# Kernel tuning notes

Measured on AMD Instinct MI355X. Metric: run time of the kernel, lower is better.

Reference implementation:

```python
import jax, jax.numpy as jnp
import numpy as np

N, E, IN, H, OUT, CD = 50000, 800000, 64, 128, 128, 2


def _lin(key, fi, fo):
    # PyTorch nn.Linear default init: U(-1/sqrt(fan_in), 1/sqrt(fan_in))
    k1, k2 = jax.random.split(key)
    s = 1.0 / np.sqrt(fi)
    W = jax.random.uniform(k1, (fi, fo), minval=-s, maxval=s, dtype=jnp.float32)
    b = jax.random.uniform(k2, (fo,), minval=-s, maxval=s, dtype=jnp.float32)
    return W, b


def setup_inputs() -> dict:
    key = jax.random.key(0)
    ks = jax.random.split(key, 12)
    feat = jax.random.normal(ks[0], (N, IN), dtype=jnp.float32)
    offsets = jax.random.normal(ks[1], (E, CD), dtype=jnp.float32)
    src = jax.random.randint(ks[2], (E,), 0, N)
    dst = jax.random.randint(ks[3], (E,), 0, N)
    kW1, kb1 = _lin(ks[4], CD, H)
    kW2, kb2 = _lin(ks[5], H, IN)
    sW1, sb1 = _lin(ks[6], IN, H)
    sW2, sb2 = _lin(ks[7], H, H)
    mW1, mb1 = _lin(ks[8], IN + H, H)
    mW2, mb2 = _lin(ks[9], H, H)
    mW3, mb3 = _lin(ks[10], H, H)
    mW4, mb4 = _lin(ks[11], H, OUT)
    return dict(feat=feat, offsets=offsets, src=src, dst=dst,
                kW1=kW1, kb1=kb1, kW2=kW2, kb2=kb2,
                sW1=sW1, sb1=sb1, sW2=sW2, sb2=sb2,
                mW1=mW1, mb1=mb1, mW2=mW2, mb2=mb2,
                mW3=mW3, mb3=mb3, mW4=mW4, mb4=mb4)


def reference(feat, offsets, src, dst, kW1, kb1, kW2, kb2, sW1, sb1, sW2, sb2,
              mW1, mb1, mW2, mb2, mW3, mb3, mW4, mb4):
    elu = jax.nn.elu
    n = feat.shape[0]
    # per-edge kernel weights from offsets: [E, IN]
    kw = elu(offsets @ kW1 + kb1) @ kW2 + kb2
    # dist_fn == 'eculidean': score = 1 / (||offsets||_1 + 0.001), edge softmax per dst node
    score = 1.0 / (jnp.sum(jnp.abs(offsets), axis=1) + 0.001)  # [E]
    mx = jax.lax.stop_gradient(jax.ops.segment_max(score, dst, num_segments=n))
    ex = jnp.exp(score - mx[dst])
    w = ex / jax.ops.segment_sum(ex, dst, num_segments=n)[dst]  # [E]
    # u_mul_e + sum aggregation: gather src feats, scale by per-edge weights, scatter-add to dst
    m = feat[src] * (w[:, None] * kw)                     # [E, IN]
    agg = jax.ops.segment_sum(m, dst, num_segments=n)     # [N, IN]
    # self branch
    h_self = elu(feat @ sW1 + sb1) @ sW2 + sb2            # [N, H]
    # concat + MLP head
    h = jnp.concatenate([agg, h_self], axis=1)            # [N, IN+H]
    h = elu(h @ mW1 + mb1)
    h = elu(h @ mW2 + mb2)
    h = elu(h @ mW3 + mb3)
    return h @ mW4 + mb4                                  # [N, OUT]
```

## Files before the change

kernel.cpp:

```cpp
#include <hip/hip_runtime.h>
#include <hip/hip_bf16.h>
#include <math.h>

#define N_NODES 50000
#define N_EDGES 800000
#define NB_SCAN ((N_NODES + 255) / 256)

typedef _Float16 half8 __attribute__((ext_vector_type(8)));
typedef _Float16 half4 __attribute__((ext_vector_type(4)));
typedef float f32x4 __attribute__((ext_vector_type(4)));

__device__ __forceinline__ float elu_f(float x) { return x > 0.f ? x : __expf(x) - 1.f; }
__device__ __forceinline__ float edge_score(float2 o) {
    return 1.f / (fabsf(o.x) + fabsf(o.y) + 0.001f);
}

__global__ __launch_bounds__(256)
void k_deg(const int* __restrict__ dst, int* __restrict__ deg) {
    int e = blockIdx.x * 256 + threadIdx.x;
    if (e >= N_EDGES) return;
    atomicAdd(&deg[dst[e]], 1);
}

__global__ __launch_bounds__(256)
void k_bsum(const int* __restrict__ deg, int* __restrict__ bsum) {
    int i = blockIdx.x * 256 + threadIdx.x;
    int v = (i < N_NODES) ? deg[i] : 0;
    #pragma unroll
    for (int d = 32; d; d >>= 1) v += __shfl_xor(v, d);
    __shared__ int ws[4];
    if ((threadIdx.x & 63) == 0) ws[threadIdx.x >> 6] = v;
    __syncthreads();
    if (threadIdx.x == 0) bsum[blockIdx.x] = ws[0] + ws[1] + ws[2] + ws[3];
}

__global__ __launch_bounds__(256)
void k_bscan(const int* __restrict__ bsum, int* __restrict__ bpre, int* __restrict__ rs) {
    const int t = threadIdx.x, lane = t & 63, wv = t >> 6;
    int v = (t < NB_SCAN) ? bsum[t] : 0;
    int inc = v;
    #pragma unroll
    for (int d = 1; d < 64; d <<= 1) { int u = __shfl_up(inc, d); if (lane >= d) inc += u; }
    __shared__ int wtot[4];
    if (lane == 63) wtot[wv] = inc;
    __syncthreads();
    int add = 0;
    for (int w = 0; w < wv; ++w) add += wtot[w];
    if (t < NB_SCAN) bpre[t] = inc + add - v;
    if (t == 0) rs[N_NODES] = N_EDGES;
}

__global__ __launch_bounds__(256)
void k_wr(const int* __restrict__ deg, const int* __restrict__ bpre,
          int* __restrict__ rs, int* __restrict__ cur) {
    const int i = blockIdx.x * 256 + threadIdx.x;
    const int lane = threadIdx.x & 63, wv = threadIdx.x >> 6;
    int v = (i < N_NODES) ? deg[i] : 0;
    int inc = v;
    #pragma unroll
    for (int d = 1; d < 64; d <<= 1) { int u = __shfl_up(inc, d); if (lane >= d) inc += u; }
    __shared__ int wtot[4];
    if (lane == 63) wtot[wv] = inc;
    __syncthreads();
    int add = bpre[blockIdx.x];
    for (int w = 0; w < wv; ++w) add += wtot[w];
    if (i < N_NODES) { int excl = inc - v + add; rs[i] = excl; cur[i] = excl; }
}

__global__ __launch_bounds__(256)
void k_fill(const int* __restrict__ dst, const int* __restrict__ src,
            const float* __restrict__ off2, int* __restrict__ cur,
            int* __restrict__ perm, int* __restrict__ src_csr,
            float* __restrict__ score_csr) {
    int e = blockIdx.x * 256 + threadIdx.x;
    if (e >= N_EDGES) return;
    int p = atomicAdd(&cur[dst[e]], 1);
    perm[e] = p;
    src_csr[p] = src[e];
    score_csr[p] = edge_score(((const float2*)off2)[e]);
}

#define WTOT 98304
__global__ __launch_bounds__(256)
void k_wsplit(const float* __restrict__ sW1, const float* __restrict__ sW2,
              const float* __restrict__ mW1, const float* __restrict__ mW2,
              const float* __restrict__ mW3, const float* __restrict__ mW4,
              _Float16* __restrict__ wsH, _Float16* __restrict__ wsL) {
    int idx = blockIdx.x * 256 + threadIdx.x;
    if (idx >= WTOT) return;
    const float* W; int base, K;
    if      (idx < 8192)  { W = sW1; base = 0;     K = 64;  }
    else if (idx < 24576) { W = sW2; base = 8192;  K = 128; }
    else if (idx < 49152) { W = mW1; base = 24576; K = 192; }
    else if (idx < 65536) { W = mW2; base = 49152; K = 128; }
    else if (idx < 81920) { W = mW3; base = 65536; K = 128; }
    else                  { W = mW4; base = 81920; K = 128; }
    int local = idx - base;
    int k = local >> 7, col = local & 127;
    int nt = col >> 4, colg = col & 15;
    int kt = k >> 5, lq = (k >> 3) & 3, i = k & 7;
    int fi = base + ((nt * (K >> 5) + kt) * 4 + lq) * 128 + colg * 8 + i;
    float w = W[k * 128 + col];
    _Float16 h = (_Float16)w;
    wsH[fi] = h;
    wsL[fi] = (_Float16)(w - (float)h);
}

#define KW2TOT 8192
__global__ __launch_bounds__(256)
void k_kwsplit2(const float* __restrict__ kW2,
                _Float16* __restrict__ wkH, _Float16* __restrict__ wkL) {
    int idx = blockIdx.x * 256 + threadIdx.x;
    if (idx >= KW2TOT) return;
    int i = idx & 7, colg = (idx >> 3) & 15;
    int lq = (idx >> 7) & 3, kt = (idx >> 9) & 3, jt = idx >> 11;
    int k = kt * 32 + lq * 8 + i;
    int j = jt * 16 + colg;
    float w = kW2[k * 64 + j];
    _Float16 h = (_Float16)w;
    wkH[idx] = h;
    wkL[idx] = (_Float16)(w - (float)h);
}

__global__ __launch_bounds__(256)
void k_kw(const float* __restrict__ off2,
          const float* __restrict__ kW1, const float* __restrict__ kb1,
          const _Float16* __restrict__ wkH, const _Float16* __restrict__ wkL,
          const float* __restrict__ kb2, const int* __restrict__ perm,
          _Float16* __restrict__ kwbuf) {
    const int t = threadIdx.x;
    const int lane = t & 63, wv = t >> 6;
    const int eb = blockIdx.x * 256 + wv * 64;
    const int colg = lane & 15, lq = lane >> 4;

    float2 o[4];
    int pidx[4];
    #pragma unroll
    for (int et = 0; et < 4; ++et) {
        o[et] = ((const float2*)off2)[eb + et * 16 + colg];
        pidx[et] = perm[eb + et * 16 + colg];
    }

    f32x4 c[4][4];
    #pragma unroll
    for (int et = 0; et < 4; ++et)
        #pragma unroll
        for (int jt = 0; jt < 4; ++jt) c[et][jt] = (f32x4){0.f, 0.f, 0.f, 0.f};

    #pragma unroll
    for (int kt = 0; kt < 4; ++kt) {
        const int k0 = kt * 32 + lq * 8;
        float4 a0 = *(const float4*)&kW1[k0];
        float4 a1 = *(const float4*)&kW1[k0 + 4];
        float4 b0 = *(const float4*)&kW1[128 + k0];
        float4 b1 = *(const float4*)&kW1[128 + k0 + 4];
        float4 c0 = *(const float4*)&kb1[k0];
        float4 c1 = *(const float4*)&kb1[k0 + 4];
        const float wa[8] = {a0.x, a0.y, a0.z, a0.w, a1.x, a1.y, a1.z, a1.w};
        const float wb[8] = {b0.x, b0.y, b0.z, b0.w, b1.x, b1.y, b1.z, b1.w};
        const float bb[8] = {c0.x, c0.y, c0.z, c0.w, c1.x, c1.y, c1.z, c1.w};

        half8 Bh[4], Bl[4];
        #pragma unroll
        for (int et = 0; et < 4; ++et) {
            #pragma unroll
            for (int i = 0; i < 8; ++i) {
                float h = elu_f(fmaf(o[et].y, wb[i], fmaf(o[et].x, wa[i], bb[i])));
                _Float16 hh = (_Float16)h;
                Bh[et][i] = hh;
                Bl[et][i] = (_Float16)(h - (float)hh);
            }
        }
        #pragma unroll
        for (int jt = 0; jt < 4; ++jt) {
            int fo = ((jt * 4 + kt) * 4 + lq) * 128 + colg * 8;
            half8 Ah = *(const half8*)&wkH[fo];
            half8 Al = *(const half8*)&wkL[fo];
            #pragma unroll
            for (int et = 0; et < 4; ++et) {
                c[et][jt] = __builtin_amdgcn_mfma_f32_16x16x32_f16(Ah, Bh[et], c[et][jt], 0, 0, 0);
                c[et][jt] = __builtin_amdgcn_mfma_f32_16x16x32_f16(Ah, Bl[et], c[et][jt], 0, 0, 0);
                c[et][jt] = __builtin_amdgcn_mfma_f32_16x16x32_f16(Al, Bh[et], c[et][jt], 0, 0, 0);
            }
        }
    }

    #pragma unroll
    for (int jt = 0; jt < 4; ++jt) {
        const int j0 = jt * 16 + lq * 4;
        float4 bv = *(const float4*)&kb2[j0];
        const float bias4[4] = {bv.x, bv.y, bv.z, bv.w};
        #pragma unroll
        for (int et = 0; et < 4; ++et) {
            half4 v;
            #pragma unroll
            for (int r = 0; r < 4; ++r) v[r] = (_Float16)(c[et][jt][r] + bias4[r]);
            *(half4*)&kwbuf[(size_t)pidx[et] * 64 + j0] = v;
        }
    }
}

__global__ __launch_bounds__(256)
void k_agg(const float* __restrict__ score_csr, const int* __restrict__ src_csr,
           const int* __restrict__ rs, const float* __restrict__ feat,
           const _Float16* __restrict__ kwbuf, float* __restrict__ agg) {
    const int lane = threadIdx.x & 63;
    const int wav  = threadIdx.x >> 6;
    const int gw   = blockIdx.x * 4 + wav;
    const int nw   = gridDim.x * 4;

    for (int n = gw; n < N_NODES; n += nw) {
        const int p0 = rs[n], p1 = rs[n + 1];
        if (p0 == p1) { agg[(size_t)n * 64 + lane] = 0.f; continue; }

        float mx = 0.f;
        for (int p = p0 + lane; p < p1; p += 64) mx = fmaxf(mx, score_csr[p]);
        #pragma unroll
        for (int d = 32; d; d >>= 1) mx = fmaxf(mx, __shfl_xor(mx, d));

        float sm = 0.f;
        for (int p = p0 + lane; p < p1; p += 64) sm += __expf(score_csr[p] - mx);
        #pragma unroll
        for (int d = 32; d; d >>= 1) sm += __shfl_xor(sm, d);
        const float dinv = 1.f / sm;

        float a0 = 0.f, a1 = 0.f, a2 = 0.f, a3 = 0.f;
        int p = p0;
        for (; p + 4 <= p1; p += 4) {
            float w0 = __expf(score_csr[p]     - mx) * dinv;
            float w1 = __expf(score_csr[p + 1] - mx) * dinv;
            float w2 = __expf(score_csr[p + 2] - mx) * dinv;
            float w3 = __expf(score_csr[p + 3] - mx) * dinv;
            const int s0 = src_csr[p], s1 = src_csr[p + 1];
            const int s2 = src_csr[p + 2], s3 = src_csr[p + 3];
            float f0 = feat[(size_t)s0 * 64 + lane];
            float f1 = feat[(size_t)s1 * 64 + lane];
            float f2 = feat[(size_t)s2 * 64 + lane];
            float f3 = feat[(size_t)s3 * 64 + lane];
            float k0 = (float)kwbuf[(size_t)(p)     * 64 + lane];
            float k1 = (float)kwbuf[(size_t)(p + 1) * 64 + lane];
            float k2 = (float)kwbuf[(size_t)(p + 2) * 64 + lane];
            float k3 = (float)kwbuf[(size_t)(p + 3) * 64 + lane];
            a0 = fmaf(f0 * w0, k0, a0);
            a1 = fmaf(f1 * w1, k1, a1);
            a2 = fmaf(f2 * w2, k2, a2);
            a3 = fmaf(f3 * w3, k3, a3);
        }
        for (; p < p1; ++p) {
            float wgt = __expf(score_csr[p] - mx) * dinv;
            float f = feat[(size_t)src_csr[p] * 64 + lane];
            float kv = (float)kwbuf[(size_t)p * 64 + lane];
            a0 = fmaf(f * wgt, kv, a0);
        }
        agg[(size_t)n * 64 + lane] = (a0 + a1) + (a2 + a3);
    }
}

__device__ __forceinline__
void mm64(const char* XH, const char* XL, const _Float16* __restrict__ WH,
          const _Float16* __restrict__ WL, int K, int lane, int wv, f32x4 c[4][2]) {
    const int colg = lane & 15, lq = lane >> 4;
    #pragma unroll
    for (int m = 0; m < 4; ++m)
        #pragma unroll
        for (int j = 0; j < 2; ++j) c[m][j] = (f32x4){0.f, 0.f, 0.f, 0.f};
    const int KT = K >> 5;
    for (int kt = 0; kt < KT; ++kt) {
        half8 Bh[2], Bl[2], Ah[4], Al[4];
        #pragma unroll
        for (int j = 0; j < 2; ++j) {
            int fo = ((((wv * 2 + j) * KT + kt) * 4 + lq) * 128) + colg * 8;
            Bh[j] = *(const half8*)&WH[fo];
            Bl[j] = *(const half8*)&WL[fo];
        }
        #pragma unroll
        for (int m = 0; m < 4; ++m) {
            int row = m * 16 + colg;
            int byte = ((row * K + kt * 32 + lq * 8) * 2) ^ ((row & 7) << 4);
            Ah[m] = *(const half8*)(XH + byte);
            Al[m] = *(const half8*)(XL + byte);
        }
        #pragma unroll
        for (int m = 0; m < 4; ++m)
            #pragma unroll
            for (int j = 0; j < 2; ++j) {
                c[m][j] = __builtin_amdgcn_mfma_f32_16x16x32_f16(Ah[m], Bh[j], c[m][j], 0, 0, 0);
                c[m][j] = __builtin_amdgcn_mfma_f32_16x16x32_f16(Ah[m], Bl[j], c[m][j], 0, 0, 0);
                c[m][j] = __builtin_amdgcn_mfma_f32_16x16x32_f16(Al[m], Bh[j], c[m][j], 0, 0, 0);
            }
    }
}

__device__ __forceinline__
void epi_lds(char* XH, char* XL, int Knext, int colOff, int lane, int wv,
             f32x4 c[4][2], const float* __restrict__ bias, bool do_elu) {
    const int colg = lane & 15, lq = lane >> 4;
    float bj[2] = { bias[wv * 32 + colg], bias[wv * 32 + 16 + colg] };
    #pragma unroll
    for (int m = 0; m < 4; ++m)
        #pragma unroll
        for (int j = 0; j < 2; ++j) {
            int col = colOff + wv * 32 + j * 16 + colg;
            #pragma unroll
            for (int r = 0; r < 4; ++r) {
                int row = m * 16 + lq * 4 + r;
                float v = c[m][j][r] + bj[j];
                if (do_elu) v = elu_f(v);
                _Float16 h = (_Float16)v;
                int byte = ((row * Knext + col) * 2) ^ ((row & 7) << 4);
                *(_Float16*)(XH + byte) = h;
                *(_Float16*)(XL + byte) = (_Float16)(v - (float)h);
            }
        }
}

__global__ __launch_bounds__(256)
void k_node(const float* __restrict__ feat, const float* __restrict__ agg,
            const _Float16* __restrict__ wsH, const _Float16* __restrict__ wsL,
            const float* __restrict__ sb1, const float* __restrict__ sb2,
            const float* __restrict__ mb1, const float* __restrict__ mb2,
            const float* __restrict__ mb3, const float* __restrict__ mb4,
            float* __restrict__ out) {
    __shared__ _Float16 XH[64 * 192];
    __shared__ _Float16 XL[64 * 192];
    const int t = threadIdx.x;
    const int lane = t & 63, wv = t >> 6;
    const int row0 = blockIdx.x * 64;
    f32x4 c[4][2];

    {
        int r = t >> 2, c4 = (t & 3) * 4;
        #pragma unroll
        for (int q = 0; q < 4; ++q) {
            int col = (c4 + q) * 4;
            float4 v = make_float4(0.f, 0.f, 0.f, 0.f);
            if (row0 + r < N_NODES) v = *(const float4*)&feat[(size_t)(row0 + r) * 64 + col];
            _Float16 h4h[4], h4l[4];
            float vv[4] = {v.x, v.y, v.z, v.w};
            #pragma unroll
            for (int i = 0; i < 4; ++i) {
                _Float16 h = (_Float16)vv[i];
                h4h[i] = h; h4l[i] = (_Float16)(vv[i] - (float)h);
            }
            int byte = ((r * 64 + col) * 2) ^ ((r & 7) << 4);
            *(ulong1*)((char*)XH + byte) = *(ulong1*)h4h;
            *(ulong1*)((char*)XL + byte) = *(ulong1*)h4l;
        }
    }
    __syncthreads();

    mm64((const char*)XH, (const char*)XL, wsH + 0, wsL + 0, 64, lane, wv, c);
    __syncthreads();
    epi_lds((char*)XH, (char*)XL, 128, 0, lane, wv, c, sb1, true);
    __syncthreads();

    mm64((const char*)XH, (const char*)XL, wsH + 8192, wsL + 8192, 128, lane, wv, c);
    __syncthreads();
    epi_lds((char*)XH, (char*)XL, 192, 64, lane, wv, c, sb2, false);
    {
        int r = t >> 2, c4 = (t & 3) * 4;
        #pragma unroll
        for (int q = 0; q < 4; ++q) {
            int col = (c4 + q) * 4;
            float4 v = make_float4(0.f, 0.f, 0.f, 0.f);
            if (row0 + r < N_NODES) v = *(const float4*)&agg[(size_t)(row0 + r) * 64 + col];
            _Float16 h4h[4], h4l[4];
            float vv[4] = {v.x, v.y, v.z, v.w};
            #pragma unroll
            for (int i = 0; i < 4; ++i) {
                _Float16 h = (_Float16)vv[i];
                h4h[i] = h; h4l[i] = (_Float16)(vv[i] - (float)h);
            }
            int byte = ((r * 192 + col) * 2) ^ ((r & 7) << 4);
            *(ulong1*)((char*)XH + byte) = *(ulong1*)h4h;
            *(ulong1*)((char*)XL + byte) = *(ulong1*)h4l;
        }
    }
    __syncthreads();

    mm64((const char*)XH, (const char*)XL, wsH + 24576, wsL + 24576, 192, lane, wv, c);
    __syncthreads();
    epi_lds((char*)XH, (char*)XL, 128, 0, lane, wv, c, mb1, true);
    __syncthreads();

    mm64((const char*)XH, (const char*)XL, wsH + 49152, wsL + 49152, 128, lane, wv, c);
    __syncthreads();
    epi_lds((char*)XH, (char*)XL, 128, 0, lane, wv, c, mb2, true);
    __syncthreads();

    mm64((const char*)XH, (const char*)XL, wsH + 65536, wsL + 65536, 128, lane, wv, c);
    __syncthreads();
    epi_lds((char*)XH, (char*)XL, 128, 0, lane, wv, c, mb3, true);
    __syncthreads();

    mm64((const char*)XH, (const char*)XL, wsH + 81920, wsL + 81920, 128, lane, wv, c);
    {
        const int colg = lane & 15, lq = lane >> 4;
        float bj[2] = { mb4[wv * 32 + colg], mb4[wv * 32 + 16 + colg] };
        #pragma unroll
        for (int m = 0; m < 4; ++m)
            #pragma unroll
            for (int j = 0; j < 2; ++j) {
                int col = wv * 32 + j * 16 + colg;
                #pragma unroll
                for (int r = 0; r < 4; ++r) {
                    int row = row0 + m * 16 + lq * 4 + r;
                    if (row < N_NODES)
                        out[(size_t)row * 128 + col] = c[m][j][r] + bj[j];
                }
            }
    }
}

extern "C" void kernel_launch(void* const* d_in, const int* in_sizes, int n_in,
                              void* d_out, int out_size, void* d_ws, size_t ws_size,
                              hipStream_t stream) {
    (void)in_sizes; (void)n_in; (void)out_size; (void)ws_size;
    const float* feat = (const float*)d_in[0];
    const float* off2 = (const float*)d_in[1];
    const int*   src  = (const int*)d_in[2];
    const int*   dst  = (const int*)d_in[3];
    const float* kW1  = (const float*)d_in[4];
    const float* kb1  = (const float*)d_in[5];
    const float* kW2  = (const float*)d_in[6];
    const float* kb2  = (const float*)d_in[7];
    const float* sW1  = (const float*)d_in[8];
    const float* sb1  = (const float*)d_in[9];
    const float* sW2  = (const float*)d_in[10];
    const float* sb2  = (const float*)d_in[11];
    const float* mW1  = (const float*)d_in[12];
    const float* mb1  = (const float*)d_in[13];
    const float* mW2  = (const float*)d_in[14];
    const float* mb2  = (const float*)d_in[15];
    const float* mW3  = (const float*)d_in[16];
    const float* mb3  = (const float*)d_in[17];
    const float* mW4  = (const float*)d_in[18];
    const float* mb4  = (const float*)d_in[19];

    char* ws = (char*)d_ws;
    size_t off = 0;
    auto alloc = [&](size_t bytes) -> void* {
        void* p = ws + off;
        off += (bytes + 255) & ~(size_t)255;
        return p;
    };
    int*   deg    = (int*)alloc((size_t)N_NODES * 4);
    int*   rs     = (int*)alloc((size_t)(N_NODES + 8) * 4);
    int*   cur    = (int*)alloc((size_t)N_NODES * 4);
    int*   bsum   = (int*)alloc((size_t)NB_SCAN * 4);
    int*   bpre   = (int*)alloc((size_t)NB_SCAN * 4);
    int*   perm   = (int*)alloc((size_t)N_EDGES * 4);
    int*   srcc   = (int*)alloc((size_t)N_EDGES * 4);
    float* scorec = (float*)alloc((size_t)N_EDGES * 4);
    float* agg    = (float*)alloc((size_t)N_NODES * 64 * 4);
    _Float16* wsH = (_Float16*)alloc((size_t)WTOT * 2);
    _Float16* wsL = (_Float16*)alloc((size_t)WTOT * 2);
    _Float16* wkH = (_Float16*)alloc((size_t)KW2TOT * 2);
    _Float16* wkL = (_Float16*)alloc((size_t)KW2TOT * 2);
    _Float16* kwbuf = (_Float16*)alloc((size_t)N_EDGES * 64 * 2);

    hipMemsetAsync(deg, 0, (size_t)N_NODES * 4, stream);

    const int EB = (N_EDGES + 255) / 256;
    const int GB = (N_NODES + 63) / 64;

    k_deg     <<<EB, 256, 0, stream>>>(dst, deg);
    k_bsum    <<<NB_SCAN, 256, 0, stream>>>(deg, bsum);
    k_bscan   <<<1, 256, 0, stream>>>(bsum, bpre, rs);
    k_wr      <<<NB_SCAN, 256, 0, stream>>>(deg, bpre, rs, cur);
    k_fill    <<<EB, 256, 0, stream>>>(dst, src, off2, cur, perm, srcc, scorec);
    k_wsplit  <<<(WTOT + 255) / 256, 256, 0, stream>>>(sW1, sW2, mW1, mW2, mW3, mW4, wsH, wsL);
    k_kwsplit2<<<(KW2TOT + 255) / 256, 256, 0, stream>>>(kW2, wkH, wkL);

    k_kw <<<N_EDGES / 256, 256, 0, stream>>>(off2, kW1, kb1, wkH, wkL, kb2, perm, kwbuf);
    k_agg<<<2048, 256, 0, stream>>>(scorec, srcc, rs, feat, kwbuf, agg);

    k_node<<<GB, 256, 0, stream>>>(feat, agg, wsH, wsL, sb1, sb2, mb1, mb2, mb3, mb4,
                                   (float*)d_out);
}
```

Measured before the change: 278.9 us.

## Use CSR edge-id gather in k_kw, merge weight-split kernels, keep agg in registers

k_fill now records the original edge id per CSR slot instead of a per-edge permutation. k_kw therefore gathers offsets through that id and writes kernel weights contiguously in CSR order, replacing scattered half4 stores with a gathered float2 load. The two weight-split kernels are merged into one launch. In k_node the aggregated features are loaded straight into MFMA operand registers for the first MLP layer, which shrinks LDS from 192 to 128 columns and drops a staging pass, at the cost of more registers.

```diff
diff --git a/kernel.cpp b/kernel.cpp
--- a/kernel.cpp
+++ b/kernel.cpp
@@ -70,76 +70,70 @@
 __global__ __launch_bounds__(256)
 void k_fill(const int* __restrict__ dst, const int* __restrict__ src,
             const float* __restrict__ off2, int* __restrict__ cur,
-            int* __restrict__ perm, int* __restrict__ src_csr,
+            int* __restrict__ eid_csr, int* __restrict__ src_csr,
             float* __restrict__ score_csr) {
     int e = blockIdx.x * 256 + threadIdx.x;
     if (e >= N_EDGES) return;
     int p = atomicAdd(&cur[dst[e]], 1);
-    perm[e] = p;
+    eid_csr[p] = e;
     src_csr[p] = src[e];
     score_csr[p] = edge_score(((const float2*)off2)[e]);
 }
 
 #define WTOT 98304
+#define KW2TOT 8192
 __global__ __launch_bounds__(256)
 void k_wsplit(const float* __restrict__ sW1, const float* __restrict__ sW2,
               const float* __restrict__ mW1, const float* __restrict__ mW2,
               const float* __restrict__ mW3, const float* __restrict__ mW4,
-              _Float16* __restrict__ wsH, _Float16* __restrict__ wsL) {
+              const float* __restrict__ kW2,
+              _Float16* __restrict__ wsH, _Float16* __restrict__ wsL,
+              _Float16* __restrict__ wkH, _Float16* __restrict__ wkL) {
     int idx = blockIdx.x * 256 + threadIdx.x;
-    if (idx >= WTOT) return;
-    const float* W; int base, K;
-    if      (idx < 8192)  { W = sW1; base = 0;     K = 64;  }
-    else if (idx < 24576) { W = sW2; base = 8192;  K = 128; }
-    else if (idx < 49152) { W = mW1; base = 24576; K = 192; }
-    else if (idx < 65536) { W = mW2; base = 49152; K = 128; }
-    else if (idx < 81920) { W = mW3; base = 65536; K = 128; }
-    else                  { W = mW4; base = 81920; K = 128; }
-    int local = idx - base;
-    int k = local >> 7, col = local & 127;
-    int nt = col >> 4, colg = col & 15;
-    int kt = k >> 5, lq = (k >> 3) & 3, i = k & 7;
-    int fi = base + ((nt * (K >> 5) + kt) * 4 + lq) * 128 + colg * 8 + i;
-    float w = W[k * 128 + col];
-    _Float16 h = (_Float16)w;
-    wsH[fi] = h;
-    wsL[fi] = (_Float16)(w - (float)h);
-}
-
-#define KW2TOT 8192
-__global__ __launch_bounds__(256)
-void k_kwsplit2(const float* __restrict__ kW2,
-                _Float16* __restrict__ wkH, _Float16* __restrict__ wkL) {
-    int idx = blockIdx.x * 256 + threadIdx.x;
-    if (idx >= KW2TOT) return;
-    int i = idx & 7, colg = (idx >> 3) & 15;
-    int lq = (idx >> 7) & 3, kt = (idx >> 9) & 3, jt = idx >> 11;
-    int k = kt * 32 + lq * 8 + i;
-    int j = jt * 16 + colg;
-    float w = kW2[k * 64 + j];
-    _Float16 h = (_Float16)w;
-    wkH[idx] = h;
-    wkL[idx] = (_Float16)(w - (float)h);
-}
-
-__global__ __launch_bounds__(256)
-void k_kw(const float* __restrict__ off2,
+    if (idx < WTOT) {
+        const float* W; int base, K;
+        if      (idx < 8192)  { W = sW1; base = 0;     K = 64;  }
+        else if (idx < 24576) { W = sW2; base = 8192;  K = 128; }
+        else if (idx < 49152) { W = mW1; base = 24576; K = 192; }
+        else if (idx < 65536) { W = mW2; base = 49152; K = 128; }
+        else if (idx < 81920) { W = mW3; base = 65536; K = 128; }
+        else                  { W = mW4; base = 81920; K = 128; }
+        int local = idx - base;
+        int k = local >> 7, col = local & 127;
+        int nt = col >> 4, colg = col & 15;
+        int kt = k >> 5, lq = (k >> 3) & 3, i = k & 7;
+        int fi = base + ((nt * (K >> 5) + kt) * 4 + lq) * 128 + colg * 8 + i;
+        float w = W[k * 128 + col];
+        _Float16 h = (_Float16)w;
+        wsH[fi] = h;
+        wsL[fi] = (_Float16)(w - (float)h);
+    } else if (idx < WTOT + KW2TOT) {
+        int x = idx - WTOT;
+        int i = x & 7, colg = (x >> 3) & 15;
+        int lq = (x >> 7) & 3, kt = (x >> 9) & 3, jt = x >> 11;
+        int k = kt * 32 + lq * 8 + i;
+        int j = jt * 16 + colg;
+        float w = kW2[k * 64 + j];
+        _Float16 h = (_Float16)w;
+        wkH[x] = h;
+        wkL[x] = (_Float16)(w - (float)h);
+    }
+}
+
+__global__ __launch_bounds__(256)
+void k_kw(const float* __restrict__ off2, const int* __restrict__ eid_csr,
           const float* __restrict__ kW1, const float* __restrict__ kb1,
           const _Float16* __restrict__ wkH, const _Float16* __restrict__ wkL,
-          const float* __restrict__ kb2, const int* __restrict__ perm,
-          _Float16* __restrict__ kwbuf) {
+          const float* __restrict__ kb2, _Float16* __restrict__ kwbuf) {
     const int t = threadIdx.x;
     const int lane = t & 63, wv = t >> 6;
-    const int eb = blockIdx.x * 256 + wv * 64;
+    const int pb = blockIdx.x * 256 + wv * 64;
     const int colg = lane & 15, lq = lane >> 4;
 
     float2 o[4];
-    int pidx[4];
-    #pragma unroll
-    for (int et = 0; et < 4; ++et) {
-        o[et] = ((const float2*)off2)[eb + et * 16 + colg];
-        pidx[et] = perm[eb + et * 16 + colg];
-    }
+    #pragma unroll
+    for (int et = 0; et < 4; ++et)
+        o[et] = ((const float2*)off2)[eid_csr[pb + et * 16 + colg]];
 
     f32x4 c[4][4];
     #pragma unroll
@@ -192,10 +186,11 @@
         const float bias4[4] = {bv.x, bv.y, bv.z, bv.w};
         #pragma unroll
         for (int et = 0; et < 4; ++et) {
+            const int p = pb + et * 16 + colg;
             half4 v;
             #pragma unroll
             for (int r = 0; r < 4; ++r) v[r] = (_Float16)(c[et][jt][r] + bias4[r]);
-            *(half4*)&kwbuf[(size_t)pidx[et] * 64 + j0] = v;
+            *(half4*)&kwbuf[(size_t)p * 64 + j0] = v;
         }
     }
 }
@@ -292,7 +287,49 @@
 }
 
 __device__ __forceinline__
-void epi_lds(char* XH, char* XL, int Knext, int colOff, int lane, int wv,
+void mm64_h1(const half8 aggH[4][2], const half8 aggL[4][2],
+             const char* XH, const char* XL,
+             const _Float16* __restrict__ WH, const _Float16* __restrict__ WL,
+             int lane, int wv, f32x4 c[4][2]) {
+    const int colg = lane & 15, lq = lane >> 4;
+    #pragma unroll
+    for (int m = 0; m < 4; ++m)
+        #pragma unroll
+        for (int j = 0; j < 2; ++j) c[m][j] = (f32x4){0.f, 0.f, 0.f, 0.f};
+    #pragma unroll
+    for (int kt = 0; kt < 6; ++kt) {
+        half8 Bh[2], Bl[2], Ah[4], Al[4];
+        #pragma unroll
+        for (int j = 0; j < 2; ++j) {
+            int fo = ((((wv * 2 + j) * 6 + kt) * 4 + lq) * 128) + colg * 8;
+            Bh[j] = *(const half8*)&WH[fo];
+            Bl[j] = *(const half8*)&WL[fo];
+        }
+        if (kt < 2) {
+            #pragma unroll
+            for (int m = 0; m < 4; ++m) { Ah[m] = aggH[m][kt]; Al[m] = aggL[m][kt]; }
+        } else {
+            #pragma unroll
+            for (int m = 0; m < 4; ++m) {
+                int row = m * 16 + colg;
+                int byte = ((row * 128 + (kt - 2) * 32 + lq * 8) * 2) ^ ((row & 7) << 4);
+                Ah[m] = *(const half8*)(XH + byte);
+                Al[m] = *(const half8*)(XL + byte);
+            }
+        }
+        #pragma unroll
+        for (int m = 0; m < 4; ++m)
+            #pragma unroll
+            for (int j = 0; j < 2; ++j) {
+                c[m][j] = __builtin_amdgcn_mfma_f32_16x16x32_f16(Ah[m], Bh[j], c[m][j], 0, 0, 0);
+                c[m][j] = __builtin_amdgcn_mfma_f32_16x16x32_f16(Ah[m], Bl[j], c[m][j], 0, 0, 0);
+                c[m][j] = __builtin_amdgcn_mfma_f32_16x16x32_f16(Al[m], Bh[j], c[m][j], 0, 0, 0);
+            }
+    }
+}
+
+__device__ __forceinline__
+void epi_lds(char* XH, char* XL, int lane, int wv,
              f32x4 c[4][2], const float* __restrict__ bias, bool do_elu) {
     const int colg = lane & 15, lq = lane >> 4;
     float bj[2] = { bias[wv * 32 + colg], bias[wv * 32 + 16 + colg] };
@@ -300,14 +337,14 @@
     for (int m = 0; m < 4; ++m)
         #pragma unroll
         for (int j = 0; j < 2; ++j) {
-            int col = colOff + wv * 32 + j * 16 + colg;
+            int col = wv * 32 + j * 16 + colg;
             #pragma unroll
             for (int r = 0; r < 4; ++r) {
                 int row = m * 16 + lq * 4 + r;
                 float v = c[m][j][r] + bj[j];
                 if (do_elu) v = elu_f(v);
                 _Float16 h = (_Float16)v;
-                int byte = ((row * Knext + col) * 2) ^ ((row & 7) << 4);
+                int byte = ((row * 128 + col) * 2) ^ ((row & 7) << 4);
                 *(_Float16*)(XH + byte) = h;
                 *(_Float16*)(XL + byte) = (_Float16)(v - (float)h);
             }
@@ -321,10 +358,11 @@
             const float* __restrict__ mb1, const float* __restrict__ mb2,
             const float* __restrict__ mb3, const float* __restrict__ mb4,
             float* __restrict__ out) {
-    __shared__ _Float16 XH[64 * 192];
-    __shared__ _Float16 XL[64 * 192];
+    __shared__ _Float16 XH[64 * 128];
+    __shared__ _Float16 XL[64 * 128];
     const int t = threadIdx.x;
     const int lane = t & 63, wv = t >> 6;
+    const int colg = lane & 15, lq = lane >> 4;
     const int row0 = blockIdx.x * 64;
     f32x4 c[4][2];
 
@@ -351,51 +389,54 @@
 
     mm64((const char*)XH, (const char*)XL, wsH + 0, wsL + 0, 64, lane, wv, c);
     __syncthreads();
-    epi_lds((char*)XH, (char*)XL, 128, 0, lane, wv, c, sb1, true);
+    epi_lds((char*)XH, (char*)XL, lane, wv, c, sb1, true);
     __syncthreads();
 
     mm64((const char*)XH, (const char*)XL, wsH + 8192, wsL + 8192, 128, lane, wv, c);
-    __syncthreads();
-    epi_lds((char*)XH, (char*)XL, 192, 64, lane, wv, c, sb2, false);
-    {
-        int r = t >> 2, c4 = (t & 3) * 4;
-        #pragma unroll
-        for (int q = 0; q < 4; ++q) {
-            int col = (c4 + q) * 4;
-            float4 v = make_float4(0.f, 0.f, 0.f, 0.f);
-            if (row0 + r < N_NODES) v = *(const float4*)&agg[(size_t)(row0 + r) * 64 + col];
-            _Float16 h4h[4], h4l[4];
-            float vv[4] = {v.x, v.y, v.z, v.w};
-            #pragma unroll
-            for (int i = 0; i < 4; ++i) {
+
+    half8 aggH[4][2], aggL[4][2];
+    #pragma unroll
+    for (int m = 0; m < 4; ++m) {
+        int row = row0 + m * 16 + colg;
+        #pragma unroll
+        for (int kt = 0; kt < 2; ++kt) {
+            int k0 = kt * 32 + lq * 8;
+            float4 v0 = make_float4(0.f, 0.f, 0.f, 0.f), v1 = v0;
+            if (row < N_NODES) {
+                v0 = *(const float4*)&agg[(size_t)row * 64 + k0];
+                v1 = *(const float4*)&agg[(size_t)row * 64 + k0 + 4];
+            }
+            float vv[8] = {v0.x, v0.y, v0.z, v0.w, v1.x, v1.y, v1.z, v1.w};
+            #pragma unroll
+            for (int i = 0; i < 8; ++i) {
                 _Float16 h = (_Float16)vv[i];
-                h4h[i] = h; h4l[i] = (_Float16)(vv[i] - (float)h);
-            }
-            int byte = ((r * 192 + col) * 2) ^ ((r & 7) << 4);
-            *(ulong1*)((char*)XH + byte) = *(ulong1*)h4h;
-            *(ulong1*)((char*)XL + byte) = *(ulong1*)h4l;
-        }
-    }
-    __syncthreads();
-
-    mm64((const char*)XH, (const char*)XL, wsH + 24576, wsL + 24576, 192, lane, wv, c);
-    __syncthreads();
-    epi_lds((char*)XH, (char*)XL, 128, 0, lane, wv, c, mb1, true);
+                aggH[m][kt][i] = h;
+                aggL[m][kt][i] = (_Float16)(vv[i] - (float)h);
+            }
+        }
+    }
+    __syncthreads();
+    epi_lds((char*)XH, (char*)XL, lane, wv, c, sb2, false);
+    __syncthreads();
+
+    mm64_h1(aggH, aggL, (const char*)XH, (const char*)XL,
+            wsH + 24576, wsL + 24576, lane, wv, c);
+    __syncthreads();
+    epi_lds((char*)XH, (char*)XL, lane, wv, c, mb1, true);
     __syncthreads();
 
     mm64((const char*)XH, (const char*)XL, wsH + 49152, wsL + 49152, 128, lane, wv, c);
     __syncthreads();
-    epi_lds((char*)XH, (char*)XL, 128, 0, lane, wv, c, mb2, true);
+    epi_lds((char*)XH, (char*)XL, lane, wv, c, mb2, true);
     __syncthreads();
 
     mm64((const char*)XH, (const char*)XL, wsH + 65536, wsL + 65536, 128, lane, wv, c);
     __syncthreads();
-    epi_lds((char*)XH, (char*)XL, 128, 0, lane, wv, c, mb3, true);
+    epi_lds((char*)XH, (char*)XL, lane, wv, c, mb3, true);
     __syncthreads();
 
     mm64((const char*)XH, (const char*)XL, wsH + 81920, wsL + 81920, 128, lane, wv, c);
     {
-        const int colg = lane & 15, lq = lane >> 4;
         float bj[2] = { mb4[wv * 32 + colg], mb4[wv * 32 + 16 + colg] };
         #pragma unroll
         for (int m = 0; m < 4; ++m)
@@ -449,7 +490,7 @@
     int*   cur    = (int*)alloc((size_t)N_NODES * 4);
     int*   bsum   = (int*)alloc((size_t)NB_SCAN * 4);
     int*   bpre   = (int*)alloc((size_t)NB_SCAN * 4);
-    int*   perm   = (int*)alloc((size_t)N_EDGES * 4);
+    int*   eidc   = (int*)alloc((size_t)N_EDGES * 4);
     int*   srcc   = (int*)alloc((size_t)N_EDGES * 4);
     float* scorec = (float*)alloc((size_t)N_EDGES * 4);
     float* agg    = (float*)alloc((size_t)N_NODES * 64 * 4);
@@ -464,15 +505,15 @@
     const int EB = (N_EDGES + 255) / 256;
     const int GB = (N_NODES + 63) / 64;
 
-    k_deg     <<<EB, 256, 0, stream>>>(dst, deg);
-    k_bsum    <<<NB_SCAN, 256, 0, stream>>>(deg, bsum);
-    k_bscan   <<<1, 256, 0, stream>>>(bsum, bpre, rs);
-    k_wr      <<<NB_SCAN, 256, 0, stream>>>(deg, bpre, rs, cur);
-    k_fill    <<<EB, 256, 0, stream>>>(dst, src, off2, cur, perm, srcc, scorec);
-    k_wsplit  <<<(WTOT + 255) / 256, 256, 0, stream>>>(sW1, sW2, mW1, mW2, mW3, mW4, wsH, wsL);
-    k_kwsplit2<<<(KW2TOT + 255) / 256, 256, 0, stream>>>(kW2, wkH, wkL);
-
-    k_kw <<<N_EDGES / 256, 256, 0, stream>>>(off2, kW1, kb1, wkH, wkL, kb2, perm, kwbuf);
+    k_deg   <<<EB, 256, 0, stream>>>(dst, deg);
+    k_bsum  <<<NB_SCAN, 256, 0, stream>>>(deg, bsum);
+    k_bscan <<<1, 256, 0, stream>>>(bsum, bpre, rs);
+    k_wr    <<<NB_SCAN, 256, 0, stream>>>(deg, bpre, rs, cur);
+    k_fill  <<<EB, 256, 0, stream>>>(dst, src, off2, cur, eidc, srcc, scorec);
+    k_wsplit<<<(WTOT + KW2TOT + 255) / 256, 256, 0, stream>>>(sW1, sW2, mW1, mW2, mW3, mW4,
+                                                              kW2, wsH, wsL, wkH, wkL);
+
+    k_kw <<<N_EDGES / 256, 256, 0, stream>>>(off2, eidc, kW1, kb1, wkH, wkL, kb2, kwbuf);
     k_agg<<<2048, 256, 0, stream>>>(scorec, srcc, rs, feat, kwbuf, agg);
 
     k_node<<<GB, 256, 0, stream>>>(feat, agg, wsH, wsL, sb1, sb2, mb1, mb2, mb3, mb4,
```

Result: no change. 279.9 us (median of 2 runs) (+0.3%).
